# Optimization experiments

Hardware: AMD Instinct MI355X
Metric: run time of the kernel (lower is better)

The kernel has to match this reference:

```python
import jax, jax.numpy as jnp
import numpy as np

DIM_IN = 768
DIM_EMB = 512
DIM_ATTN = 384
N_EXPERTS = 13
TOP_K = 5
NUM_CLS = 2
K_INST = 100000  # instances per bag (WSI patches)


def setup_inputs() -> dict:
    key = jax.random.key(0)
    ks = jax.random.split(key, 10)
    s = 0.02  # weight init scale
    return {
        "X_tfl": jax.random.normal(ks[0], (1, N_EXPERTS, DIM_EMB), jnp.float32),
        "X": jax.random.normal(ks[1], (1, K_INST, DIM_IN), jnp.float32),
        # feat_proj: Linear(dim_in, dim_emb) + ReLU (end_with_fc=False, eval -> no dropout)
        "W_proj": (jax.random.normal(ks[2], (DIM_IN, DIM_EMB), jnp.float32) * s),
        "b_proj": jnp.zeros((DIM_EMB,), jnp.float32),
        # Attn_Net: Linear(L,D) -> Tanh -> Linear(D,1)
        "W_attn1": (jax.random.normal(ks[3], (DIM_EMB, DIM_ATTN), jnp.float32) * s),
        "b_attn1": jnp.zeros((DIM_ATTN,), jnp.float32),
        "W_attn2": (jax.random.normal(ks[4], (DIM_ATTN, 1), jnp.float32) * s),
        "b_attn2": jnp.zeros((1,), jnp.float32),
        # router: Linear(dim_emb, n_experts, bias=False)
        "W_router": (jax.random.normal(ks[5], (DIM_EMB, N_EXPERTS), jnp.float32) * s),
        # pred_head: Linear(dim_emb, num_cls)
        "W_pred": (jax.random.normal(ks[6], (DIM_EMB, NUM_CLS), jnp.float32) * s),
        "b_pred": jnp.zeros((NUM_CLS,), jnp.float32),
    }


def reference(X_tfl, X, W_proj, b_proj, W_attn1, b_attn1, W_attn2, b_attn2,
              W_router, W_pred, b_pred):
    # feat_proj (eval mode: dropout is identity)
    H = jax.nn.relu(jnp.einsum('bkc,cd->bkd', X, W_proj) + b_proj)  # [1,K,512]
    # attention pooling (Attn_Net): tanh MLP -> scalar score per instance
    scores = jnp.einsum('bkd,de->bke', jnp.tanh(H @ W_attn1 + b_attn1), W_attn2) + b_attn2  # [1,K,1]
    A = jax.nn.softmax(scores[..., 0], axis=-1)      # [1,K]
    M = jnp.einsum('bk,bkd->bd', A, H)               # [1,512] slide representation
    # router + top-k gating
    router_logits = M @ W_router                     # [1,13]
    probs = jax.nn.softmax(router_logits, axis=-1)
    weights, sel_idx = jax.lax.top_k(probs, TOP_K)   # [1,5], [1,5]
    # Identity experts: expert i output is X_tfl[0, i, :]; gather selected, weighted combine
    sel = X_tfl[0][sel_idx[0]]                       # [5,512]
    moe_output = jnp.sum(weights[0][:, None] * sel, axis=0)[None, :]  # [1,512]
    logit = moe_output @ W_pred + b_pred             # [1,2]
    return logit
```

## Files before the change

kernel.cpp:

```cpp
#include <hip/hip_runtime.h>
#include <hip/hip_bf16.h>

typedef __attribute__((ext_vector_type(8))) short short8_t;
typedef __attribute__((ext_vector_type(4))) float f32x4;
typedef __attribute__((ext_vector_type(4))) unsigned int u32x4;

#define KINST 100000
#define KPAD  100096
#define DIMIN 768
#define DIMEMB 512
#define DIMATTN 384

__device__ __forceinline__ unsigned short f2bf(float f) {
    unsigned int u = __builtin_bit_cast(unsigned int, f);
    u = u + 0x7FFFu + ((u >> 16) & 1u);
    return (unsigned short)(u >> 16);
}
__device__ __forceinline__ unsigned int packbf(float a, float b) {
    return (unsigned int)f2bf(a) | ((unsigned int)f2bf(b) << 16);
}
__device__ __forceinline__ float bf2f(unsigned short h) {
    unsigned int u = ((unsigned int)h) << 16;
    return __builtin_bit_cast(float, u);
}
__device__ __forceinline__ float fast_tanh(float x) {
    const float e2 = __expf(2.f * x);
    return (e2 - 1.f) * __builtin_amdgcn_rcpf(e2 + 1.f);
}

__global__ __launch_bounds__(256) void k_prep(
    const float* __restrict__ Wproj, const float* __restrict__ W1,
    unsigned short* __restrict__ WpTt, unsigned short* __restrict__ W1Tt)
{
    const int idx = blockIdx.x * 256 + threadIdx.x;
    if (idx < 49152) {
        const int t = idx >> 11, r = idx & 2047;
        const int n = r >> 2, c = r & 3;
        short8_t v;
        #pragma unroll
        for (int e = 0; e < 8; ++e)
            v[e] = (short)f2bf(Wproj[(size_t)(t * 32 + c * 8 + e) * DIMEMB + n]);
        *(short8_t*)&WpTt[t * 16384 + n * 32 + c * 8] = v;
    } else {
        const int j = idx - 49152;
        const int t = j / 3072, r = j % 3072;
        const int n = r >> 3, c = r & 7;
        short8_t v;
        #pragma unroll
        for (int e = 0; e < 8; ++e)
            v[e] = (short)f2bf(W1[(size_t)(t * 64 + c * 8 + e) * DIMATTN + n]);
        *(short8_t*)&W1Tt[t * 24576 + n * 64 + c * 8] = v;
    }
}

__global__ __launch_bounds__(256, 2) void k_gemm1(
    const float* __restrict__ X,
    const unsigned short* __restrict__ WpTt,
    const float* __restrict__ bproj,
    unsigned short* __restrict__ H)
{
    __shared__ unsigned short As[2][2048];
    const int tid = threadIdx.x;
    const int lane = tid & 63, w = tid >> 6;
    const int g = lane >> 4, fr = lane & 15;
    const int brow = blockIdx.x * 64;

    const int arow = tid >> 2, aq4 = tid & 3;
    int agr = brow + arow; if (agr >= KINST) agr = KINST - 1;
    const float* xsrc = X + (size_t)agr * DIMIN + aq4 * 8;
    const int awoff = arow * 32 + ((aq4 ^ ((arow >> 1) & 3)) << 3);
    const int aro = (g ^ ((fr >> 1) & 3)) << 3;

    const unsigned short* gB = WpTt + (size_t)(w * 128 + fr) * 32 + g * 8;

    f32x4 acc[4][8] = {};
    short8_t Bf[8];
    float4 xv[2][2];

    {
        float4 xa = *(const float4*)(xsrc);
        float4 xb = *(const float4*)(xsrc + 4);
        xv[1][0] = *(const float4*)(xsrc + 32);
        xv[1][1] = *(const float4*)(xsrc + 36);
        u32x4 p;
        p[0] = packbf(xa.x, xa.y); p[1] = packbf(xa.z, xa.w);
        p[2] = packbf(xb.x, xb.y); p[3] = packbf(xb.z, xb.w);
        *(u32x4*)&As[0][awoff] = p;
    }
    asm volatile("s_waitcnt lgkmcnt(0)" ::: "memory");
    __builtin_amdgcn_sched_barrier(0);
    __builtin_amdgcn_s_barrier();
    __builtin_amdgcn_sched_barrier(0);

#define G1STEP(P, T)                                                           \
    {                                                                          \
                  \
        const unsigned short* gBt = gB + (size_t)(T) * 16384;                  \
        _Pragma("unroll")                                                      \
        for (int j = 0; j < 8; ++j)                                            \
            Bf[j] = *(const short8_t*)(gBt + j * 512);                         \
                                                       \
        short8_t af[4];                                                        \
        _Pragma("unroll")                                                      \
        for (int i = 0; i < 4; ++i)                                            \
            af[i] = *(const short8_t*)&As[P][(i * 16 + fr) * 32 + aro];        \
        if ((T) < 23) {               \
            u32x4 p;                                                           \
            p[0] = packbf(xv[(P) ^ 1][0].x, xv[(P) ^ 1][0].y);                 \
            p[1] = packbf(xv[(P) ^ 1][0].z, xv[(P) ^ 1][0].w);                 \
            p[2] = packbf(xv[(P) ^ 1][1].x, xv[(P) ^ 1][1].y);                 \
            p[3] = packbf(xv[(P) ^ 1][1].z, xv[(P) ^ 1][1].w);                 \
            *(u32x4*)&As[(P) ^ 1][awoff] = p;                                  \
        }                                                                      \
        if ((T) < 22) {          \
            xv[P][0] = *(const float4*)(xsrc + ((T) + 2) * 32);                \
            xv[P][1] = *(const float4*)(xsrc + ((T) + 2) * 32 + 4);            \
        }                                                                      \
        if ((T) < 23) {                                                        \
            asm volatile("s_waitcnt lgkmcnt(0)" ::: "memory");                 \
            __builtin_amdgcn_sched_barrier(0);                                 \
            __builtin_amdgcn_s_barrier();                                      \
            __builtin_amdgcn_sched_barrier(0);                                 \
        }                                                                      \
        __builtin_amdgcn_s_setprio(1);                                        \
        _Pragma("unroll")                                                      \
        for (int j = 0; j < 8; ++j)                                            \
            _Pragma("unroll")                                                  \
            for (int i = 0; i < 4; ++i)                                        \
                acc[i][j] = __builtin_amdgcn_mfma_f32_16x16x32_bf16(           \
                    af[i], Bf[j], acc[i][j], 0, 0, 0);                         \
        __builtin_amdgcn_s_setprio(0);                                        \
    }

    for (int tt = 0; tt < 24; tt += 2) {
        G1STEP(0, tt);
        G1STEP(1, tt + 1);
    }
#undef G1STEP

    #pragma unroll
    for (int j = 0; j < 8; ++j) {
        const int col = w * 128 + j * 16 + fr;
        const float bias = bproj[col];
        #pragma unroll
        for (int i = 0; i < 4; ++i) {
            const int rb = brow + i * 16 + g * 4;
            #pragma unroll
            for (int r = 0; r < 4; ++r) {
                const int row = rb + r;
                const float v = fmaxf(acc[i][j][r] + bias, 0.f);
                H[(size_t)row * DIMEMB + col] = (row < KINST) ? f2bf(v) : (unsigned short)0;
            }
        }
    }
}

__global__ __launch_bounds__(256, 2) void k_gemm2(
    const unsigned short* __restrict__ H,
    const unsigned short* __restrict__ W1Tt,
    const float* __restrict__ b1,
    const float* __restrict__ W2,
    float* __restrict__ Tpart)
{
    __shared__ float sred[2][128];
    const int tid = threadIdx.x;
    const int lane = tid & 63, w = tid >> 6;
    const int wr = w >> 1, wc = w & 1;
    const int g = lane >> 4, fr = lane & 15;
    const int cb = blockIdx.x;
    const int brow = blockIdx.y * 128;
    const int bcol = cb * 128;

    const unsigned short* gA = H + (size_t)(brow + wr * 64 + fr) * DIMEMB + g * 8;
    const unsigned short* gB = W1Tt + (size_t)(bcol + wc * 64 + fr) * 64 + g * 8;

    f32x4 acc[4][4] = {};
    short8_t Af[2][8], Bf[2][8];

    #pragma unroll
    for (int i = 0; i < 4; ++i)
        #pragma unroll
        for (int kk = 0; kk < 2; ++kk)
            Af[0][i * 2 + kk] = *(const short8_t*)(gA + (size_t)i * 8192 + kk * 32);
    #pragma unroll
    for (int j = 0; j < 4; ++j)
        #pragma unroll
        for (int kk = 0; kk < 2; ++kk)
            Bf[0][j * 2 + kk] = *(const short8_t*)(gB + (size_t)j * 1024 + kk * 32);

    #pragma unroll
    for (int t = 0; t < 8; ++t) {
        const int b = t & 1;
        if (t < 7) {
            const unsigned short* gAt = gA + (size_t)(t + 1) * 64;
            const unsigned short* gBt = gB + (size_t)(t + 1) * 24576;
            #pragma unroll
            for (int i = 0; i < 4; ++i)
                #pragma unroll
                for (int kk = 0; kk < 2; ++kk)
                    Af[b ^ 1][i * 2 + kk] = *(const short8_t*)(gAt + (size_t)i * 8192 + kk * 32);
            #pragma unroll
            for (int j = 0; j < 4; ++j)
                #pragma unroll
                for (int kk = 0; kk < 2; ++kk)
                    Bf[b ^ 1][j * 2 + kk] = *(const short8_t*)(gBt + (size_t)j * 1024 + kk * 32);
        }
        __builtin_amdgcn_s_setprio(1);
        #pragma unroll
        for (int kk = 0; kk < 2; ++kk)
            #pragma unroll
            for (int j = 0; j < 4; ++j)
                #pragma unroll
                for (int i = 0; i < 4; ++i)
                    acc[i][j] = __builtin_amdgcn_mfma_f32_16x16x32_bf16(
                        Af[b][i * 2 + kk], Bf[b][j * 2 + kk], acc[i][j], 0, 0, 0);
        __builtin_amdgcn_s_setprio(0);
    }

    float ps[4][4] = {};
    #pragma unroll
    for (int j = 0; j < 4; ++j) {
        const int col = bcol + wc * 64 + j * 16 + fr;
        const float bb = b1[col], ww = W2[col];
        #pragma unroll
        for (int i = 0; i < 4; ++i)
            #pragma unroll
            for (int r = 0; r < 4; ++r)
                ps[i][r] += fast_tanh(acc[i][j][r] + bb) * ww;
    }
    #pragma unroll
    for (int off = 1; off < 16; off <<= 1)
        #pragma unroll
        for (int i = 0; i < 4; ++i)
            #pragma unroll
            for (int r = 0; r < 4; ++r)
                ps[i][r] += __shfl_xor(ps[i][r], off, 64);
    if (fr == 0) {
        #pragma unroll
        for (int i = 0; i < 4; ++i)
            #pragma unroll
            for (int r = 0; r < 4; ++r)
                sred[wc][wr * 64 + i * 16 + g * 4 + r] = ps[i][r];
    }
    __syncthreads();
    if (tid < 128)
        Tpart[(size_t)cb * KPAD + brow + tid] = sred[0][tid] + sred[1][tid];
}

__global__ __launch_bounds__(512) void k_poolE(
    const float* __restrict__ Tpart,
    const unsigned short* __restrict__ H,
    const float* __restrict__ b2,
    float* __restrict__ Spart,
    float* __restrict__ Mpart)
{
    __shared__ float Elds[1024];
    __shared__ float red[8][512];
    __shared__ float ssum[8];
    const int tid = threadIdx.x, lane = tid & 63, w = tid >> 6;
    const int base = blockIdx.x * 1024;
    const float bb = b2[0];
    float es = 0.f;
    #pragma unroll
    for (int u = 0; u < 2; ++u) {
        const int r = base + u * 512 + tid;
        float e = 0.f;
        if (r < KINST)
            e = __expf(Tpart[r] + Tpart[KPAD + r] + Tpart[2 * KPAD + r] + bb);
        Elds[u * 512 + tid] = e;
        es += e;
    }
    #pragma unroll
    for (int off = 1; off < 64; off <<= 1) es += __shfl_xor(es, off, 64);
    if (lane == 0) ssum[w] = es;
    __syncthreads();
    if (tid == 0) {
        float t = 0.f;
        #pragma unroll
        for (int i = 0; i < 8; ++i) t += ssum[i];
        Spart[blockIdx.x] = t;
    }

    float pa[8] = {};
    for (int i = 0; i < 128; ++i) {
        const int lr = i * 8 + w;
        const float e = Elds[lr];
        if (e != 0.f) {
            const int r = base + lr;
            const short8_t v = *(const short8_t*)(H + (size_t)r * DIMEMB + lane * 8);
            #pragma unroll
            for (int j = 0; j < 8; ++j) pa[j] += e * bf2f((unsigned short)v[j]);
        }
    }
    #pragma unroll
    for (int j = 0; j < 8; ++j) red[w][lane * 8 + j] = pa[j];
    __syncthreads();
    float s2 = 0.f;
    #pragma unroll
    for (int k = 0; k < 8; ++k) s2 += red[k][tid];
    Mpart[(size_t)blockIdx.x * DIMEMB + tid] = s2;
}

__global__ __launch_bounds__(512) void k_head(
    const float* __restrict__ Spart,
    const float* __restrict__ Mpart,
    const float* __restrict__ Wr,
    const float* __restrict__ Xtfl,
    const float* __restrict__ Wp,
    const float* __restrict__ bp,
    float* __restrict__ outp)
{
    __shared__ float Mlds[512];
    __shared__ float logits[13];
    __shared__ float wsel[5];
    __shared__ int isel[5];
    __shared__ float Slds;
    __shared__ float swred[8];
    __shared__ float r0s[8], r1s[8];
    const int tid = threadIdx.x, lane = tid & 63, w = tid >> 6;

    float s = 0.f;
    if (tid < 98) s = Spart[tid];
    #pragma unroll
    for (int off = 1; off < 64; off <<= 1) s += __shfl_xor(s, off, 64);
    if (lane == 0) swred[w] = s;

    float m = 0.f;
    #pragma unroll 2
    for (int b = 0; b < 98; ++b) m += Mpart[(size_t)b * 512 + tid];

    __syncthreads();
    if (tid == 0) {
        float t = 0.f;
        #pragma unroll
        for (int i = 0; i < 8; ++i) t += swred[i];
        Slds = t;
    }
    __syncthreads();
    Mlds[tid] = m / Slds;
    __syncthreads();
    if (tid < 13) {
        float l = 0.f;
        for (int dd = 0; dd < 512; ++dd) l += Mlds[dd] * Wr[dd * 13 + tid];
        logits[tid] = l;
    }
    __syncthreads();
    if (tid == 0) {
        float mx = -1e30f;
        for (int i = 0; i < 13; ++i) mx = fmaxf(mx, logits[i]);
        float pe[13]; float sum = 0.f;
        for (int i = 0; i < 13; ++i) { pe[i] = __expf(logits[i] - mx); sum += pe[i]; }
        unsigned used = 0;
        for (int t = 0; t < 5; ++t) {
            int bi = 0; float bv = -1.f;
            for (int i = 0; i < 13; ++i)
                if (!((used >> i) & 1u) && pe[i] > bv) { bv = pe[i]; bi = i; }
            used |= (1u << bi);
            wsel[t] = bv / sum;
            isel[t] = bi;
        }
    }
    __syncthreads();
    float mo = 0.f;
    #pragma unroll
    for (int t = 0; t < 5; ++t) mo += wsel[t] * Xtfl[isel[t] * 512 + tid];
    float p0 = mo * Wp[tid * 2 + 0];
    float p1 = mo * Wp[tid * 2 + 1];
    #pragma unroll
    for (int off = 1; off < 64; off <<= 1) {
        p0 += __shfl_xor(p0, off, 64);
        p1 += __shfl_xor(p1, off, 64);
    }
    if (lane == 0) { r0s[w] = p0; r1s[w] = p1; }
    __syncthreads();
    if (tid == 0) {
        float a = bp[0], b = bp[1];
        for (int i = 0; i < 8; ++i) { a += r0s[i]; b += r1s[i]; }
        outp[0] = a; outp[1] = b;
    }
}

extern "C" void kernel_launch(void* const* d_in, const int* in_sizes, int n_in,
                              void* d_out, int out_size, void* d_ws, size_t ws_size,
                              hipStream_t stream)
{
    const float* Xtfl  = (const float*)d_in[0];
    const float* X     = (const float*)d_in[1];
    const float* Wproj = (const float*)d_in[2];
    const float* bproj = (const float*)d_in[3];
    const float* W1    = (const float*)d_in[4];
    const float* b1    = (const float*)d_in[5];
    const float* W2    = (const float*)d_in[6];
    const float* b2    = (const float*)d_in[7];
    const float* Wr    = (const float*)d_in[8];
    const float* Wp    = (const float*)d_in[9];
    const float* bp    = (const float*)d_in[10];
    float* out = (float*)d_out;

    char* ws = (char*)d_ws;
    size_t off = 0;
    unsigned short* H    = (unsigned short*)(ws + off); off += (size_t)KPAD * DIMEMB * 2;
    unsigned short* WpTt = (unsigned short*)(ws + off); off += (size_t)DIMEMB * DIMIN * 2;
    unsigned short* W1Tt = (unsigned short*)(ws + off); off += (size_t)DIMATTN * DIMEMB * 2;
    float* Tpart = (float*)(ws + off); off += (size_t)3 * KPAD * 4;
    float* Spart = (float*)(ws + off); off += 1024;
    float* Mpart = (float*)(ws + off); off += (size_t)98 * DIMEMB * 4;

    k_prep<<<288, 256, 0, stream>>>(Wproj, W1, WpTt, W1Tt);
    k_gemm1<<<1564, 256, 0, stream>>>(X, WpTt, bproj, H);
    k_gemm2<<<dim3(3, 782), 256, 0, stream>>>(H, W1Tt, b1, W2, Tpart);
    k_poolE<<<98, 512, 0, stream>>>(Tpart, H, b2, Spart, Mpart);
    k_head<<<1, 512, 0, stream>>>(Spart, Mpart, Wr, Xtfl, Wp, bp, out);
}
```

Measured before the change: 401.1 us.

## Fuse attention scoring with softmax pooling and split gemm1 across column halves

The second GEMM now handles 128 rows across the full 384 attention width with 512 threads. It computes the exp-scores and the weighted H partial sums in the same kernel, which removes the separate pooling kernel and the Tpart round trip. Its A tile is staged into LDS with global_load_lds double buffering. The first GEMM is split into two column blocks of 256 per row tile, giving a smaller accumulator and more occupancy at the cost of reading and converting X twice. The head kernel now reduces 782 partial rows with 1024 threads.

```diff
diff --git a/kernel.cpp b/kernel.cpp
--- a/kernel.cpp
+++ b/kernel.cpp
@@ -26,6 +26,11 @@
 __device__ __forceinline__ float fast_tanh(float x) {
     const float e2 = __expf(2.f * x);
     return (e2 - 1.f) * __builtin_amdgcn_rcpf(e2 + 1.f);
+}
+__device__ __forceinline__ void gll16(const unsigned short* g, unsigned short* l) {
+    __builtin_amdgcn_global_load_lds(
+        (const __attribute__((address_space(1))) unsigned int*)g,
+        (__attribute__((address_space(3))) unsigned int*)l, 16, 0, 0);
 }
 
 __global__ __launch_bounds__(256) void k_prep(
@@ -53,7 +58,7 @@
     }
 }
 
-__global__ __launch_bounds__(256, 2) void k_gemm1(
+__global__ __launch_bounds__(256, 4) void k_gemm1(
     const float* __restrict__ X,
     const unsigned short* __restrict__ WpTt,
     const float* __restrict__ bproj,
@@ -63,7 +68,8 @@
     const int tid = threadIdx.x;
     const int lane = tid & 63, w = tid >> 6;
     const int g = lane >> 4, fr = lane & 15;
-    const int brow = blockIdx.x * 64;
+    const int bcol = blockIdx.x * 256;
+    const int brow = blockIdx.y * 64;
 
     const int arow = tid >> 2, aq4 = tid & 3;
     int agr = brow + arow; if (agr >= KINST) agr = KINST - 1;
@@ -71,17 +77,16 @@
     const int awoff = arow * 32 + ((aq4 ^ ((arow >> 1) & 3)) << 3);
     const int aro = (g ^ ((fr >> 1) & 3)) << 3;
 
-    const unsigned short* gB = WpTt + (size_t)(w * 128 + fr) * 32 + g * 8;
-
-    f32x4 acc[4][8] = {};
-    short8_t Bf[8];
-    float4 xv[2][2];
+    const unsigned short* gB = WpTt + (size_t)(bcol + w * 64 + fr) * 32 + g * 8;
+
+    f32x4 acc[4][4] = {};
+    float4 xva, xvb;
 
     {
         float4 xa = *(const float4*)(xsrc);
         float4 xb = *(const float4*)(xsrc + 4);
-        xv[1][0] = *(const float4*)(xsrc + 32);
-        xv[1][1] = *(const float4*)(xsrc + 36);
+        xva = *(const float4*)(xsrc + 32);
+        xvb = *(const float4*)(xsrc + 36);
         u32x4 p;
         p[0] = packbf(xa.x, xa.y); p[1] = packbf(xa.z, xa.w);
         p[2] = packbf(xb.x, xb.y); p[3] = packbf(xb.z, xb.w);
@@ -94,10 +99,11 @@
 
 #define G1STEP(P, T)                                                           \
     {                                                                          \
-                  \
+                        \
         const unsigned short* gBt = gB + (size_t)(T) * 16384;                  \
+        short8_t Bf[4];                                                        \
         _Pragma("unroll")                                                      \
-        for (int j = 0; j < 8; ++j)                                            \
+        for (int j = 0; j < 4; ++j)                                            \
             Bf[j] = *(const short8_t*)(gBt + j * 512);                         \
                                                        \
         short8_t af[4];                                                        \
@@ -106,15 +112,13 @@
             af[i] = *(const short8_t*)&As[P][(i * 16 + fr) * 32 + aro];        \
         if ((T) < 23) {               \
             u32x4 p;                                                           \
-            p[0] = packbf(xv[(P) ^ 1][0].x, xv[(P) ^ 1][0].y);                 \
-            p[1] = packbf(xv[(P) ^ 1][0].z, xv[(P) ^ 1][0].w);                 \
-            p[2] = packbf(xv[(P) ^ 1][1].x, xv[(P) ^ 1][1].y);                 \
-            p[3] = packbf(xv[(P) ^ 1][1].z, xv[(P) ^ 1][1].w);                 \
+            p[0] = packbf(xva.x, xva.y); p[1] = packbf(xva.z, xva.w);          \
+            p[2] = packbf(xvb.x, xvb.y); p[3] = packbf(xvb.z, xvb.w);          \
             *(u32x4*)&As[(P) ^ 1][awoff] = p;                                  \
         }                                                                      \
-        if ((T) < 22) {          \
-            xv[P][0] = *(const float4*)(xsrc + ((T) + 2) * 32);                \
-            xv[P][1] = *(const float4*)(xsrc + ((T) + 2) * 32 + 4);            \
+        if ((T) < 22) {                   \
+            xva = *(const float4*)(xsrc + ((T) + 2) * 32);                     \
+            xvb = *(const float4*)(xsrc + ((T) + 2) * 32 + 4);                 \
         }                                                                      \
         if ((T) < 23) {                                                        \
             asm volatile("s_waitcnt lgkmcnt(0)" ::: "memory");                 \
@@ -124,7 +128,7 @@
         }                                                                      \
         __builtin_amdgcn_s_setprio(1);                                        \
         _Pragma("unroll")                                                      \
-        for (int j = 0; j < 8; ++j)                                            \
+        for (int j = 0; j < 4; ++j)                                            \
             _Pragma("unroll")                                                  \
             for (int i = 0; i < 4; ++i)                                        \
                 acc[i][j] = __builtin_amdgcn_mfma_f32_16x16x32_bf16(           \
@@ -139,8 +143,8 @@
 #undef G1STEP
 
     #pragma unroll
-    for (int j = 0; j < 8; ++j) {
-        const int col = w * 128 + j * 16 + fr;
+    for (int j = 0; j < 4; ++j) {
+        const int col = bcol + w * 64 + j * 16 + fr;
         const float bias = bproj[col];
         #pragma unroll
         for (int i = 0; i < 4; ++i) {
@@ -155,72 +159,70 @@
     }
 }
 
-__global__ __launch_bounds__(256, 2) void k_gemm2(
+__global__ __launch_bounds__(512, 2) void k_gemm2(
     const unsigned short* __restrict__ H,
     const unsigned short* __restrict__ W1Tt,
     const float* __restrict__ b1,
     const float* __restrict__ W2,
-    float* __restrict__ Tpart)
+    const float* __restrict__ b2,
+    float* __restrict__ Spart,
+    float* __restrict__ Mpart)
 {
-    __shared__ float sred[2][128];
+    __shared__ unsigned short As[2][4096];
+    __shared__ float sred[4][128];
+    __shared__ float Elds[128];
+    __shared__ float ssum[8];
+    __shared__ float red[8][512];
     const int tid = threadIdx.x;
     const int lane = tid & 63, w = tid >> 6;
-    const int wr = w >> 1, wc = w & 1;
+    const int wr = w >> 2, wc = w & 3;
     const int g = lane >> 4, fr = lane & 15;
-    const int cb = blockIdx.x;
-    const int brow = blockIdx.y * 128;
-    const int bcol = cb * 128;
-
-    const unsigned short* gA = H + (size_t)(brow + wr * 64 + fr) * DIMEMB + g * 8;
-    const unsigned short* gB = W1Tt + (size_t)(bcol + wc * 64 + fr) * 64 + g * 8;
-
-    f32x4 acc[4][4] = {};
-    short8_t Af[2][8], Bf[2][8];
-
-    #pragma unroll
-    for (int i = 0; i < 4; ++i)
-        #pragma unroll
-        for (int kk = 0; kk < 2; ++kk)
-            Af[0][i * 2 + kk] = *(const short8_t*)(gA + (size_t)i * 8192 + kk * 32);
-    #pragma unroll
-    for (int j = 0; j < 4; ++j)
-        #pragma unroll
-        for (int kk = 0; kk < 2; ++kk)
-            Bf[0][j * 2 + kk] = *(const short8_t*)(gB + (size_t)j * 1024 + kk * 32);
-
-    #pragma unroll
-    for (int t = 0; t < 8; ++t) {
-        const int b = t & 1;
-        if (t < 7) {
-            const unsigned short* gAt = gA + (size_t)(t + 1) * 64;
-            const unsigned short* gBt = gB + (size_t)(t + 1) * 24576;
+    const int brow = blockIdx.x * 128;
+
+    const int sr = w * 16 + (lane >> 2);
+    const int c_src = (lane & 3) ^ ((sr >> 1) & 3);
+    const unsigned short* gA = H + (size_t)(brow + sr) * DIMEMB + c_src * 8;
+    unsigned short* ldst0 = &As[0][w * 512 + lane * 8];
+    unsigned short* ldst1 = &As[1][w * 512 + lane * 8];
+    const int aro = (g ^ ((fr >> 1) & 3)) << 3;
+
+    const unsigned short* gB = W1Tt + (size_t)(wc * 96 + fr) * 64 + g * 8;
+
+    f32x4 acc[4][6] = {};
+
+    gll16(gA, ldst0);
+    asm volatile("s_waitcnt vmcnt(0)" ::: "memory");
+    __builtin_amdgcn_s_barrier();
+
+    for (int t = 0; t < 16; ++t) {
+        const int buf = t & 1;
+        if (t < 15) gll16(gA + (t + 1) * 32, buf ? ldst0 : ldst1);
+        short8_t Bf[6];
+        const unsigned short* gBt = gB + (size_t)(t >> 1) * 24576 + (t & 1) * 32;
+        #pragma unroll
+        for (int j = 0; j < 6; ++j)
+            Bf[j] = *(const short8_t*)(gBt + j * 1024);
+        short8_t af[4];
+        #pragma unroll
+        for (int i = 0; i < 4; ++i)
+            af[i] = *(const short8_t*)&As[buf][(wr * 64 + i * 16 + fr) * 32 + aro];
+        __builtin_amdgcn_s_setprio(1);
+        #pragma unroll
+        for (int j = 0; j < 6; ++j)
             #pragma unroll
             for (int i = 0; i < 4; ++i)
-                #pragma unroll
-                for (int kk = 0; kk < 2; ++kk)
-                    Af[b ^ 1][i * 2 + kk] = *(const short8_t*)(gAt + (size_t)i * 8192 + kk * 32);
-            #pragma unroll
-            for (int j = 0; j < 4; ++j)
-                #pragma unroll
-                for (int kk = 0; kk < 2; ++kk)
-                    Bf[b ^ 1][j * 2 + kk] = *(const short8_t*)(gBt + (size_t)j * 1024 + kk * 32);
+                acc[i][j] = __builtin_amdgcn_mfma_f32_16x16x32_bf16(af[i], Bf[j], acc[i][j], 0, 0, 0);
+        __builtin_amdgcn_s_setprio(0);
+        if (t < 15) {
+            asm volatile("s_waitcnt vmcnt(0) lgkmcnt(0)" ::: "memory");
+            __builtin_amdgcn_s_barrier();
         }
-        __builtin_amdgcn_s_setprio(1);
-        #pragma unroll
-        for (int kk = 0; kk < 2; ++kk)
-            #pragma unroll
-            for (int j = 0; j < 4; ++j)
-                #pragma unroll
-                for (int i = 0; i < 4; ++i)
-                    acc[i][j] = __builtin_amdgcn_mfma_f32_16x16x32_bf16(
-                        Af[b][i * 2 + kk], Bf[b][j * 2 + kk], acc[i][j], 0, 0, 0);
-        __builtin_amdgcn_s_setprio(0);
     }
 
     float ps[4][4] = {};
     #pragma unroll
-    for (int j = 0; j < 4; ++j) {
-        const int col = bcol + wc * 64 + j * 16 + fr;
+    for (int j = 0; j < 6; ++j) {
+        const int col = wc * 96 + j * 16 + fr;
         const float bb = b1[col], ww = W2[col];
         #pragma unroll
         for (int i = 0; i < 4; ++i)
@@ -243,57 +245,39 @@
                 sred[wc][wr * 64 + i * 16 + g * 4 + r] = ps[i][r];
     }
     __syncthreads();
-    if (tid < 128)
-        Tpart[(size_t)cb * KPAD + brow + tid] = sred[0][tid] + sred[1][tid];
-}
-
-__global__ __launch_bounds__(512) void k_poolE(
-    const float* __restrict__ Tpart,
-    const unsigned short* __restrict__ H,
-    const float* __restrict__ b2,
-    float* __restrict__ Spart,
-    float* __restrict__ Mpart)
-{
-    __shared__ float Elds[1024];
-    __shared__ float red[8][512];
-    __shared__ float ssum[8];
-    const int tid = threadIdx.x, lane = tid & 63, w = tid >> 6;
-    const int base = blockIdx.x * 1024;
-    const float bb = b2[0];
-    float es = 0.f;
-    #pragma unroll
-    for (int u = 0; u < 2; ++u) {
-        const int r = base + u * 512 + tid;
-        float e = 0.f;
-        if (r < KINST)
-            e = __expf(Tpart[r] + Tpart[KPAD + r] + Tpart[2 * KPAD + r] + bb);
-        Elds[u * 512 + tid] = e;
-        es += e;
-    }
-    #pragma unroll
-    for (int off = 1; off < 64; off <<= 1) es += __shfl_xor(es, off, 64);
-    if (lane == 0) ssum[w] = es;
+    float myE = 0.f;
+    if (tid < 128) {
+        const int row = brow + tid;
+        const float s = sred[0][tid] + sred[1][tid] + sred[2][tid] + sred[3][tid] + b2[0];
+        const float e = __expf(s);
+        const float eg = (row < KINST) ? e : 0.f;
+        Elds[tid] = eg;
+        myE = eg;
+    }
+    #pragma unroll
+    for (int off = 1; off < 64; off <<= 1) myE += __shfl_xor(myE, off, 64);
+    if (lane == 0) ssum[w] = myE;
     __syncthreads();
     if (tid == 0) {
-        float t = 0.f;
-        #pragma unroll
-        for (int i = 0; i < 8; ++i) t += ssum[i];
-        Spart[blockIdx.x] = t;
+        float tacc = 0.f;
+        #pragma unroll
+        for (int i = 0; i < 8; ++i) tacc += ssum[i];
+        Spart[blockIdx.x] = tacc;
     }
 
     float pa[8] = {};
-    for (int i = 0; i < 128; ++i) {
-        const int lr = i * 8 + w;
-        const float e = Elds[lr];
-        if (e != 0.f) {
-            const int r = base + lr;
-            const short8_t v = *(const short8_t*)(H + (size_t)r * DIMEMB + lane * 8);
-            #pragma unroll
-            for (int j = 0; j < 8; ++j) pa[j] += e * bf2f((unsigned short)v[j]);
-        }
-    }
-    #pragma unroll
-    for (int j = 0; j < 8; ++j) red[w][lane * 8 + j] = pa[j];
+    const int hb = lane << 3;
+    #pragma unroll 4
+    for (int i = 0; i < 16; ++i) {
+        const int r = (w << 4) + i;
+        const float e = Elds[r];
+        const short8_t v = *(const short8_t*)(H + (size_t)(brow + r) * DIMEMB + hb);
+        #pragma unroll
+        for (int j = 0; j < 8; ++j)
+            pa[j] += e * bf2f((unsigned short)v[j]);
+    }
+    #pragma unroll
+    for (int j = 0; j < 8; ++j) red[w][hb + j] = pa[j];
     __syncthreads();
     float s2 = 0.f;
     #pragma unroll
@@ -301,7 +285,7 @@
     Mpart[(size_t)blockIdx.x * DIMEMB + tid] = s2;
 }
 
-__global__ __launch_bounds__(512) void k_head(
+__global__ __launch_bounds__(1024) void k_head(
     const float* __restrict__ Spart,
     const float* __restrict__ Mpart,
     const float* __restrict__ Wr,
@@ -311,33 +295,38 @@
     float* __restrict__ outp)
 {
     __shared__ float Mlds[512];
+    __shared__ float red2[2][512];
     __shared__ float logits[13];
     __shared__ float wsel[5];
     __shared__ int isel[5];
     __shared__ float Slds;
-    __shared__ float swred[8];
-    __shared__ float r0s[8], r1s[8];
+    __shared__ float swred[16];
+    __shared__ float r0s[16], r1s[16];
     const int tid = threadIdx.x, lane = tid & 63, w = tid >> 6;
+    const int half = tid >> 9, d = tid & 511;
 
     float s = 0.f;
-    if (tid < 98) s = Spart[tid];
+    for (int i = tid; i < 782; i += 1024) s += Spart[i];
     #pragma unroll
     for (int off = 1; off < 64; off <<= 1) s += __shfl_xor(s, off, 64);
     if (lane == 0) swred[w] = s;
 
     float m = 0.f;
-    #pragma unroll 2
-    for (int b = 0; b < 98; ++b) m += Mpart[(size_t)b * 512 + tid];
+    #pragma unroll 4
+    for (int b = half; b < 782; b += 2) m += Mpart[(size_t)b * 512 + d];
+    red2[half][d] = m;
 
     __syncthreads();
     if (tid == 0) {
         float t = 0.f;
         #pragma unroll
-        for (int i = 0; i < 8; ++i) t += swred[i];
+        for (int i = 0; i < 16; ++i) t += swred[i];
         Slds = t;
     }
     __syncthreads();
-    Mlds[tid] = m / Slds;
+    if (tid < 512) {
+        Mlds[tid] = (red2[0][tid] + red2[1][tid]) / Slds;
+    }
     __syncthreads();
     if (tid < 13) {
         float l = 0.f;
@@ -361,11 +350,14 @@
         }
     }
     __syncthreads();
-    float mo = 0.f;
-    #pragma unroll
-    for (int t = 0; t < 5; ++t) mo += wsel[t] * Xtfl[isel[t] * 512 + tid];
-    float p0 = mo * Wp[tid * 2 + 0];
-    float p1 = mo * Wp[tid * 2 + 1];
+    float p0 = 0.f, p1 = 0.f;
+    if (tid < 512) {
+        float mo = 0.f;
+        #pragma unroll
+        for (int t = 0; t < 5; ++t) mo += wsel[t] * Xtfl[isel[t] * 512 + tid];
+        p0 = mo * Wp[tid * 2 + 0];
+        p1 = mo * Wp[tid * 2 + 1];
+    }
     #pragma unroll
     for (int off = 1; off < 64; off <<= 1) {
         p0 += __shfl_xor(p0, off, 64);
@@ -375,7 +367,7 @@
     __syncthreads();
     if (tid == 0) {
         float a = bp[0], b = bp[1];
-        for (int i = 0; i < 8; ++i) { a += r0s[i]; b += r1s[i]; }
+        for (int i = 0; i < 16; ++i) { a += r0s[i]; b += r1s[i]; }
         outp[0] = a; outp[1] = b;
     }
 }
@@ -402,13 +394,11 @@
     unsigned short* H    = (unsigned short*)(ws + off); off += (size_t)KPAD * DIMEMB * 2;
     unsigned short* WpTt = (unsigned short*)(ws + off); off += (size_t)DIMEMB * DIMIN * 2;
     unsigned short* W1Tt = (unsigned short*)(ws + off); off += (size_t)DIMATTN * DIMEMB * 2;
-    float* Tpart = (float*)(ws + off); off += (size_t)3 * KPAD * 4;
-    float* Spart = (float*)(ws + off); off += 1024;
-    float* Mpart = (float*)(ws + off); off += (size_t)98 * DIMEMB * 4;
+    float* Spart = (float*)(ws + off); off += 4096;
+    float* Mpart = (float*)(ws + off); off += (size_t)782 * DIMEMB * 4;
 
     k_prep<<<288, 256, 0, stream>>>(Wproj, W1, WpTt, W1Tt);
-    k_gemm1<<<1564, 256, 0, stream>>>(X, WpTt, bproj, H);
-    k_gemm2<<<dim3(3, 782), 256, 0, stream>>>(H, W1Tt, b1, W2, Tpart);
-    k_poolE<<<98, 512, 0, stream>>>(Tpart, H, b2, Spart, Mpart);
-    k_head<<<1, 512, 0, stream>>>(Spart, Mpart, Wr, Xtfl, Wp, bp, out);
-}
+    k_gemm1<<<dim3(2, 1564), 256, 0, stream>>>(X, WpTt, bproj, H);
+    k_gemm2<<<782, 512, 0, stream>>>(H, W1Tt, b1, W2, b2, Spart, Mpart);
+    k_head<<<1, 1024, 0, stream>>>(Spart, Mpart, Wr, Xtfl, Wp, bp, out);
+}
```

After: 382.3 us. 1.05x faster.

## Stage gemm2 tiles via global_load_lds with XOR-swizzled H and W1 layouts

Applied to the files above, without the earlier changes.

k_gemm2 now copies A (H) and B (W1) tiles from global memory straight into double-buffered LDS using global_load_lds, replacing per-wave register loads, and reads MFMA fragments from LDS. H and W1 are stored with an XOR column swizzle so the LDS fragment reads avoid bank conflicts, and the gemm1 epilogue and pooling reader are updated to match that layout. gemm1 also double-buffers its B-fragment register loads one step ahead. The cost is more LDS use and a barrier per k-step in gemm2, which lowers occupancy, plus higher register pressure in gemm1.

```diff
diff --git a/kernel.cpp b/kernel.cpp
--- a/kernel.cpp
+++ b/kernel.cpp
@@ -27,10 +27,15 @@
     const float e2 = __expf(2.f * x);
     return (e2 - 1.f) * __builtin_amdgcn_rcpf(e2 + 1.f);
 }
+__device__ __forceinline__ void gll16(const unsigned short* g, unsigned short* l) {
+    __builtin_amdgcn_global_load_lds(
+        (const __attribute__((address_space(1))) unsigned int*)g,
+        (__attribute__((address_space(3))) unsigned int*)l, 16, 0, 0);
+}
 
 __global__ __launch_bounds__(256) void k_prep(
     const float* __restrict__ Wproj, const float* __restrict__ W1,
-    unsigned short* __restrict__ WpTt, unsigned short* __restrict__ W1Tt)
+    unsigned short* __restrict__ WpTt, unsigned short* __restrict__ W1Ts)
 {
     const int idx = blockIdx.x * 256 + threadIdx.x;
     if (idx < 49152) {
@@ -44,12 +49,12 @@
     } else {
         const int j = idx - 49152;
         const int t = j / 3072, r = j % 3072;
-        const int n = r >> 3, c = r & 7;
+        const int c = r / 384, n = r % 384;
         short8_t v;
         #pragma unroll
         for (int e = 0; e < 8; ++e)
             v[e] = (short)f2bf(W1[(size_t)(t * 64 + c * 8 + e) * DIMATTN + n]);
-        *(short8_t*)&W1Tt[t * 24576 + n * 64 + c * 8] = v;
+        *(short8_t*)&W1Ts[t * 24576 + n * 64 + ((c ^ (n & 7)) << 3)] = v;
     }
 }
 
@@ -74,14 +79,17 @@
     const unsigned short* gB = WpTt + (size_t)(w * 128 + fr) * 32 + g * 8;
 
     f32x4 acc[4][8] = {};
-    short8_t Bf[8];
-    float4 xv[2][2];
+    short8_t Bf[2][8];
+    float4 xva, xvb;
 
     {
         float4 xa = *(const float4*)(xsrc);
         float4 xb = *(const float4*)(xsrc + 4);
-        xv[1][0] = *(const float4*)(xsrc + 32);
-        xv[1][1] = *(const float4*)(xsrc + 36);
+        #pragma unroll
+        for (int j = 0; j < 8; ++j)
+            Bf[0][j] = *(const short8_t*)(gB + j * 512);
+        xva = *(const float4*)(xsrc + 32);
+        xvb = *(const float4*)(xsrc + 36);
         u32x4 p;
         p[0] = packbf(xa.x, xa.y); p[1] = packbf(xa.z, xa.w);
         p[2] = packbf(xb.x, xb.y); p[3] = packbf(xb.z, xb.w);
@@ -94,41 +102,37 @@
 
 #define G1STEP(P, T)                                                           \
     {                                                                          \
-                  \
-        const unsigned short* gBt = gB + (size_t)(T) * 16384;                  \
-        _Pragma("unroll")                                                      \
-        for (int j = 0; j < 8; ++j)                                            \
-            Bf[j] = *(const short8_t*)(gBt + j * 512);                         \
-                                                       \
-        short8_t af[4];                                                        \
+        if ((T) < 23) {       \
+            const unsigned short* gBt = gB + (size_t)((T) + 1) * 16384;        \
+            _Pragma("unroll")                                                  \
+            for (int j = 0; j < 8; ++j)                                        \
+                Bf[(P) ^ 1][j] = *(const short8_t*)(gBt + j * 512);            \
+        }                                                                      \
+        short8_t af[4];                      \
         _Pragma("unroll")                                                      \
         for (int i = 0; i < 4; ++i)                                            \
             af[i] = *(const short8_t*)&As[P][(i * 16 + fr) * 32 + aro];        \
-        if ((T) < 23) {               \
+        if ((T) < 23) {                     \
             u32x4 p;                                                           \
-            p[0] = packbf(xv[(P) ^ 1][0].x, xv[(P) ^ 1][0].y);                 \
-            p[1] = packbf(xv[(P) ^ 1][0].z, xv[(P) ^ 1][0].w);                 \
-            p[2] = packbf(xv[(P) ^ 1][1].x, xv[(P) ^ 1][1].y);                 \
-            p[3] = packbf(xv[(P) ^ 1][1].z, xv[(P) ^ 1][1].w);                 \
+            p[0] = packbf(xva.x, xva.y); p[1] = packbf(xva.z, xva.w);          \
+            p[2] = packbf(xvb.x, xvb.y); p[3] = packbf(xvb.z, xvb.w);          \
             *(u32x4*)&As[(P) ^ 1][awoff] = p;                                  \
         }                                                                      \
-        if ((T) < 22) {          \
-            xv[P][0] = *(const float4*)(xsrc + ((T) + 2) * 32);                \
-            xv[P][1] = *(const float4*)(xsrc + ((T) + 2) * 32 + 4);            \
+        if ((T) < 22) {                   \
+            xva = *(const float4*)(xsrc + ((T) + 2) * 32);                     \
+            xvb = *(const float4*)(xsrc + ((T) + 2) * 32 + 4);                 \
         }                                                                      \
-        if ((T) < 23) {                                                        \
-            asm volatile("s_waitcnt lgkmcnt(0)" ::: "memory");                 \
-            __builtin_amdgcn_sched_barrier(0);                                 \
-            __builtin_amdgcn_s_barrier();                                      \
-            __builtin_amdgcn_sched_barrier(0);                                 \
-        }                                                                      \
+        asm volatile("s_waitcnt lgkmcnt(0)" ::: "memory");                     \
+        __builtin_amdgcn_sched_barrier(0);                                     \
+        __builtin_amdgcn_s_barrier();                                          \
+        __builtin_amdgcn_sched_barrier(0);                                     \
         __builtin_amdgcn_s_setprio(1);                                        \
         _Pragma("unroll")                                                      \
         for (int j = 0; j < 8; ++j)                                            \
             _Pragma("unroll")                                                  \
             for (int i = 0; i < 4; ++i)                                        \
                 acc[i][j] = __builtin_amdgcn_mfma_f32_16x16x32_bf16(           \
-                    af[i], Bf[j], acc[i][j], 0, 0, 0);                         \
+                    af[i], Bf[P][j], acc[i][j], 0, 0, 0);                      \
         __builtin_amdgcn_s_setprio(0);                                        \
     }
 
@@ -142,6 +146,7 @@
     for (int j = 0; j < 8; ++j) {
         const int col = w * 128 + j * 16 + fr;
         const float bias = bproj[col];
+        const int tile = (col >> 6) << 6, cc = (col >> 3) & 7, lo = col & 7;
         #pragma unroll
         for (int i = 0; i < 4; ++i) {
             const int rb = brow + i * 16 + g * 4;
@@ -149,19 +154,22 @@
             for (int r = 0; r < 4; ++r) {
                 const int row = rb + r;
                 const float v = fmaxf(acc[i][j][r] + bias, 0.f);
-                H[(size_t)row * DIMEMB + col] = (row < KINST) ? f2bf(v) : (unsigned short)0;
+                H[(size_t)row * DIMEMB + tile + ((cc ^ (row & 7)) << 3) + lo] =
+                    (row < KINST) ? f2bf(v) : (unsigned short)0;
             }
         }
     }
 }
 
-__global__ __launch_bounds__(256, 2) void k_gemm2(
+__global__ __launch_bounds__(256) void k_gemm2(
     const unsigned short* __restrict__ H,
-    const unsigned short* __restrict__ W1Tt,
+    const unsigned short* __restrict__ W1Ts,
     const float* __restrict__ b1,
     const float* __restrict__ W2,
     float* __restrict__ Tpart)
 {
+    __shared__ unsigned short As[2][8192];
+    __shared__ unsigned short Bs[2][8192];
     __shared__ float sred[2][128];
     const int tid = threadIdx.x;
     const int lane = tid & 63, w = tid >> 6;
@@ -171,50 +179,48 @@
     const int brow = blockIdx.y * 128;
     const int bcol = cb * 128;
 
-    const unsigned short* gA = H + (size_t)(brow + wr * 64 + fr) * DIMEMB + g * 8;
-    const unsigned short* gB = W1Tt + (size_t)(bcol + wc * 64 + fr) * 64 + g * 8;
+    const unsigned short* gA = H + (size_t)(brow + w * 32 + (lane >> 3)) * DIMEMB + (lane & 7) * 8;
+    const unsigned short* gB = W1Ts + (size_t)(bcol + w * 32 + (lane >> 3)) * 64 + (lane & 7) * 8;
+    const int loff = w * 2048 + lane * 8;
 
     f32x4 acc[4][4] = {};
-    short8_t Af[2][8], Bf[2][8];
-
-    #pragma unroll
-    for (int i = 0; i < 4; ++i)
-        #pragma unroll
-        for (int kk = 0; kk < 2; ++kk)
-            Af[0][i * 2 + kk] = *(const short8_t*)(gA + (size_t)i * 8192 + kk * 32);
-    #pragma unroll
-    for (int j = 0; j < 4; ++j)
-        #pragma unroll
-        for (int kk = 0; kk < 2; ++kk)
-            Bf[0][j * 2 + kk] = *(const short8_t*)(gB + (size_t)j * 1024 + kk * 32);
-
-    #pragma unroll
+
+    #pragma unroll
+    for (int q = 0; q < 4; ++q) {
+        gll16(gA + q * 4096, &As[0][loff + q * 512]);
+        gll16(gB + q * 512,  &Bs[0][loff + q * 512]);
+    }
+    __syncthreads();
+
     for (int t = 0; t < 8; ++t) {
-        const int b = t & 1;
+        const int buf = t & 1;
         if (t < 7) {
-            const unsigned short* gAt = gA + (size_t)(t + 1) * 64;
-            const unsigned short* gBt = gB + (size_t)(t + 1) * 24576;
-            #pragma unroll
-            for (int i = 0; i < 4; ++i)
-                #pragma unroll
-                for (int kk = 0; kk < 2; ++kk)
-                    Af[b ^ 1][i * 2 + kk] = *(const short8_t*)(gAt + (size_t)i * 8192 + kk * 32);
-            #pragma unroll
-            for (int j = 0; j < 4; ++j)
-                #pragma unroll
-                for (int kk = 0; kk < 2; ++kk)
-                    Bf[b ^ 1][j * 2 + kk] = *(const short8_t*)(gBt + (size_t)j * 1024 + kk * 32);
+            #pragma unroll
+            for (int q = 0; q < 4; ++q) {
+                gll16(gA + (t + 1) * 64 + q * 4096,           &As[buf ^ 1][loff + q * 512]);
+                gll16(gB + (size_t)(t + 1) * 24576 + q * 512, &Bs[buf ^ 1][loff + q * 512]);
+            }
         }
         __builtin_amdgcn_s_setprio(1);
         #pragma unroll
-        for (int kk = 0; kk < 2; ++kk)
-            #pragma unroll
-            for (int j = 0; j < 4; ++j)
+        for (int kk = 0; kk < 2; ++kk) {
+            short8_t af[4];
+            #pragma unroll
+            for (int i = 0; i < 4; ++i) {
+                const int row = wr * 64 + i * 16 + fr;
+                af[i] = *(const short8_t*)&As[buf][row * 64 + (((kk * 4 + g) ^ (fr & 7)) << 3)];
+            }
+            #pragma unroll
+            for (int j = 0; j < 4; ++j) {
+                const int rowb = wc * 64 + j * 16 + fr;
+                const short8_t bf = *(const short8_t*)&Bs[buf][rowb * 64 + (((kk * 4 + g) ^ (fr & 7)) << 3)];
                 #pragma unroll
                 for (int i = 0; i < 4; ++i)
-                    acc[i][j] = __builtin_amdgcn_mfma_f32_16x16x32_bf16(
-                        Af[b][i * 2 + kk], Bf[b][j * 2 + kk], acc[i][j], 0, 0, 0);
+                    acc[i][j] = __builtin_amdgcn_mfma_f32_16x16x32_bf16(af[i], bf, acc[i][j], 0, 0, 0);
+            }
+        }
         __builtin_amdgcn_s_setprio(0);
+        if (t < 7) __syncthreads();
     }
 
     float ps[4][4] = {};
@@ -282,12 +288,13 @@
     }
 
     float pa[8] = {};
+    const int tile = (lane >> 3) << 6, cf = lane & 7;
     for (int i = 0; i < 128; ++i) {
         const int lr = i * 8 + w;
         const float e = Elds[lr];
         if (e != 0.f) {
             const int r = base + lr;
-            const short8_t v = *(const short8_t*)(H + (size_t)r * DIMEMB + lane * 8);
+            const short8_t v = *(const short8_t*)(H + (size_t)r * DIMEMB + tile + ((cf ^ (r & 7)) << 3));
             #pragma unroll
             for (int j = 0; j < 8; ++j) pa[j] += e * bf2f((unsigned short)v[j]);
         }
@@ -401,14 +408,14 @@
     size_t off = 0;
     unsigned short* H    = (unsigned short*)(ws + off); off += (size_t)KPAD * DIMEMB * 2;
     unsigned short* WpTt = (unsigned short*)(ws + off); off += (size_t)DIMEMB * DIMIN * 2;
-    unsigned short* W1Tt = (unsigned short*)(ws + off); off += (size_t)DIMATTN * DIMEMB * 2;
+    unsigned short* W1Ts = (unsigned short*)(ws + off); off += (size_t)DIMATTN * DIMEMB * 2;
     float* Tpart = (float*)(ws + off); off += (size_t)3 * KPAD * 4;
     float* Spart = (float*)(ws + off); off += 1024;
     float* Mpart = (float*)(ws + off); off += (size_t)98 * DIMEMB * 4;
 
-    k_prep<<<288, 256, 0, stream>>>(Wproj, W1, WpTt, W1Tt);
+    k_prep<<<288, 256, 0, stream>>>(Wproj, W1, WpTt, W1Ts);
     k_gemm1<<<1564, 256, 0, stream>>>(X, WpTt, bproj, H);
-    k_gemm2<<<dim3(3, 782), 256, 0, stream>>>(H, W1Tt, b1, W2, Tpart);
+    k_gemm2<<<dim3(3, 782), 256, 0, stream>>>(H, W1Ts, b1, W2, Tpart);
     k_poolE<<<98, 512, 0, stream>>>(Tpart, H, b2, Spart, Mpart);
     k_head<<<1, 512, 0, stream>>>(Spart, Mpart, Wr, Xtfl, Wp, bp, out);
 }
```

Result: faster. 329.1 us (-17.9%).
